# Optimization experiments

Measured on AMD Instinct MI355X. Metric: run time of the kernel, lower is better.

Reference implementation:

```python
import jax, jax.numpy as jnp
import numpy as np
import math

N_EMBED = 8192
EMBD_DIM = 256
B, T = 16, 1024
LN_EPS = 1e-5


def setup_inputs() -> dict:
    key = jax.random.key(0)
    k1, k2 = jax.random.split(key)
    return {
        "input": jax.random.normal(k1, (B, T, EMBD_DIM), dtype=jnp.float32),
        "ln_w": jnp.ones((EMBD_DIM,), dtype=jnp.float32),
        "ln_b": jnp.zeros((EMBD_DIM,), dtype=jnp.float32),
        "embd": jax.random.normal(k2, (N_EMBED, EMBD_DIM), dtype=jnp.float32),
    }


def reference(input, ln_w, ln_b, embd):
    # LayerNorm over last dim (eps matches torch default 1e-5)
    mean = jnp.mean(input, axis=-1, keepdims=True)
    var = jnp.mean(jnp.square(input - mean), axis=-1, keepdims=True)
    x = (input - mean) * jax.lax.rsqrt(var + LN_EPS) * ln_w + ln_b
    # attention-style soft quantization: Q=x, K=V=embd
    scale = 1.0 / math.sqrt(EMBD_DIM)
    logits = jnp.einsum('btd,nd->btn', x, embd) * scale  # [B,T,N]
    probs = jax.nn.softmax(logits, axis=-1)
    idxs = jnp.argmax(probs, axis=-1)  # [B,T]
    quantize = jnp.einsum('btn,nd->btd', probs, embd)  # [B,T,D]
    return (quantize, idxs)
```

## Files before the change

### kernel.cpp

```cpp
#include <hip/hip_runtime.h>
#include <stdint.h>

#define N_EMB 8192
#define M_TOT 16384
#define DELTA 6e-3f
#define LN_EPS 1e-5f
#define SCL 0.09016994f

typedef _Float16 f16;
typedef f16 f16x8 __attribute__((ext_vector_type(8)));
typedef f16 f16x4 __attribute__((ext_vector_type(4)));
typedef float f32x16 __attribute__((ext_vector_type(16)));
typedef unsigned uint32x4 __attribute__((ext_vector_type(4)));

#define WS_KFRAG 0ul
#define WS_VFRAG (4ul << 20)
#define WS_COUNT (8ul << 20)
#define WS_LIST ((8ul << 20) + 64ul)
#define WS_PART (9ul << 20)
#define WS_EMBDT (10ul << 20)

#define MFMA32(a, b, c) __builtin_amdgcn_mfma_f32_32x32x16_f16(a, b, c, 0, 0, 0)
#define SBAR() __builtin_amdgcn_sched_barrier(0)

__global__ __launch_bounds__(256) void prep_kernel(const float* __restrict__ embd,
                                                   f16* __restrict__ kfrag,
                                                   f16* __restrict__ vfrag,
                                                   float* __restrict__ embd_t,
                                                   unsigned* __restrict__ count) {
  const int t = threadIdx.x;
  const int bid = blockIdx.x;
  if (bid < 256) {
    if (bid == 0 && t == 0) *count = 0u;
    __shared__ f16 tile[32][272];
    const int c = bid;
    {
      const int r = t >> 3;
      const int d0 = (t & 7) * 32;
      const float4* src = (const float4*)(embd + (size_t)(c * 32 + r) * 256 + d0);
#pragma unroll
      for (int qd = 0; qd < 8; ++qd) {
        float4 v = src[qd];
        tile[r][d0 + qd * 4 + 0] = (f16)v.x;
        tile[r][d0 + qd * 4 + 1] = (f16)v.y;
        tile[r][d0 + qd * 4 + 2] = (f16)v.z;
        tile[r][d0 + qd * 4 + 3] = (f16)v.w;
      }
    }
    __syncthreads();
#pragma unroll
    for (int i = 0; i < 4; ++i) {
      const int u = t + i * 256;
      const int kc = u >> 6;
      const int l = u & 63;
      const f16x8 pack = *(const f16x8*)&tile[l & 31][kc * 16 + ((l >> 5) & 1) * 8];
      *(f16x8*)(kfrag + (size_t)c * 8192 + (size_t)u * 8) = pack;
    }
#pragma unroll
    for (int i = 0; i < 4; ++i) {
      const int u = t + i * 256;
      const int fi = u >> 6;
      const int l = u & 63;
      const int dt = fi >> 1, ks = fi & 1;
      f16x8 pack;
#pragma unroll
      for (int j = 0; j < 8; ++j)
        pack[j] = tile[ks * 16 + ((l >> 5) & 1) * 8 + j][dt * 32 + (l & 31)];
      *(f16x8*)(vfrag + (size_t)c * 8192 + (size_t)u * 8) = pack;
    }
  } else {
    __shared__ float ftile[32][257];
    const int c = bid - 256;
    {
      const int r = t >> 3;
      const int d0 = (t & 7) * 32;
      const float4* src = (const float4*)(embd + (size_t)(c * 32 + r) * 256 + d0);
#pragma unroll
      for (int q8 = 0; q8 < 8; ++q8) {
        const float4 v = src[q8];
        ftile[r][d0 + q8 * 4 + 0] = v.x;
        ftile[r][d0 + q8 * 4 + 1] = v.y;
        ftile[r][d0 + q8 * 4 + 2] = v.z;
        ftile[r][d0 + q8 * 4 + 3] = v.w;
      }
    }
    __syncthreads();
    const int r = t & 31;
    const int dh = t >> 5;
#pragma unroll
    for (int dd = 0; dd < 32; ++dd) {
      const int d = dd * 8 + dh;
      embd_t[(size_t)d * 8192 + c * 32 + r] = ftile[r][d];
    }
  }
}

__global__ __launch_bounds__(256, 2) void fused_kernel(
    const float* __restrict__ input, const float* __restrict__ ln_w,
    const float* __restrict__ ln_b, const f16* __restrict__ kfrag,
    const f16* __restrict__ vfrag, float* __restrict__ out_q,
    float* __restrict__ out_idx, unsigned* __restrict__ count,
    int* __restrict__ list) {
  __shared__ __align__(16) char lds[36864];
  const int tid = threadIdx.x;
  const int lane = tid & 63;
  const int w = tid >> 6;
  const int q = lane & 31;
  const int hi = lane >> 5;
  const int R0 = blockIdx.x * 32;

  const f16* const kfbase = kfrag + (size_t)(w * 64) * 8192 + (size_t)lane * 8;
  const f16* const vfbase = vfrag + (size_t)(w * 64) * 8192 + (size_t)lane * 8;
  const char* const qb = lds + hi * 512 + q * 16;

  f16x8 kA[8];
#pragma unroll
  for (int f = 0; f < 8; ++f) kA[f] = *(const f16x8*)(kfbase + f * 512);

  {
    const int r = tid >> 3;
    const int seg = tid & 7;
    const float* rowp = input + (size_t)(R0 + r) * 256 + seg * 32;
    float4 xv[8];
    float sm = 0.f, ssq = 0.f;
#pragma unroll
    for (int qd = 0; qd < 8; ++qd) {
      xv[qd] = ((const float4*)rowp)[qd];
      sm += xv[qd].x + xv[qd].y + xv[qd].z + xv[qd].w;
      ssq += xv[qd].x * xv[qd].x + xv[qd].y * xv[qd].y + xv[qd].z * xv[qd].z +
             xv[qd].w * xv[qd].w;
    }
    sm += __shfl_xor(sm, 1);
    sm += __shfl_xor(sm, 2);
    sm += __shfl_xor(sm, 4);
    ssq += __shfl_xor(ssq, 1);
    ssq += __shfl_xor(ssq, 2);
    ssq += __shfl_xor(ssq, 4);
    const float mean = sm * (1.f / 256.f);
    const float var = ssq * (1.f / 256.f) - mean * mean;
    const float rstd = 1.0f / sqrtf(var + LN_EPS);
#pragma unroll
    for (int qd = 0; qd < 8; ++qd) {
      const int d0 = seg * 32 + qd * 4;
      float4 w4 = *(const float4*)(ln_w + d0);
      float4 b4 = *(const float4*)(ln_b + d0);
      f16x4 hv;
      hv[0] = (f16)((((xv[qd].x - mean) * rstd) * w4.x + b4.x) * SCL);
      hv[1] = (f16)((((xv[qd].y - mean) * rstd) * w4.y + b4.y) * SCL);
      hv[2] = (f16)((((xv[qd].z - mean) * rstd) * w4.z + b4.z) * SCL);
      hv[3] = (f16)((((xv[qd].w - mean) * rstd) * w4.w + b4.w) * SCL);
      const int off = (d0 >> 4) * 1024 + ((d0 >> 3) & 1) * 512 + r * 16 + (d0 & 7) * 2;
      *(f16x4*)(lds + off) = hv;
    }
  }
  __syncthreads();

  f32x16 acc[8] = {};
  float m_run = 0.f, l_run = 0.f, mt1 = -3.0e38f, mt2 = -3.0e38f;
  int i1 = 0;

  for (int c = 0; c < 64; ++c) {
    const int nb = w * 2048 + c * 32;
    const f16* const kc_base = kfbase + (size_t)c * 8192;
    const f16* const vc_base = vfbase + (size_t)c * 8192;
    SBAR();
    __builtin_amdgcn_s_barrier();
    SBAR();
    f16x8 kB[8];
#pragma unroll
    for (int f = 0; f < 8; ++f) kB[f] = *(const f16x8*)(kc_base + 4096 + f * 512);
    f32x16 S = {};
#pragma unroll
    for (int kc = 0; kc < 8; ++kc) {
      const f16x8 qf = *(const f16x8*)(qb + kc * 1024);
      S = MFMA32(kA[kc], qf, S);
    }
    f16x8 va[8];
#pragma unroll
    for (int dt = 0; dt < 8; ++dt) va[dt] = *(const f16x8*)(vc_base + dt * 1024);
#pragma unroll
    for (int kc = 0; kc < 8; ++kc) {
      const f16x8 qf = *(const f16x8*)(qb + (8 + kc) * 1024);
      S = MFMA32(kB[kc], qf, S);
    }
    f16x8 vb[8];
#pragma unroll
    for (int dt = 0; dt < 8; ++dt)
      vb[dt] = *(const f16x8*)(vc_base + 512 + dt * 1024);

    const float y0 = fmaxf(fmaxf(S[0], S[1]), fmaxf(S[2], S[3]));
    const float y1 = fmaxf(fmaxf(S[4], S[5]), fmaxf(S[6], S[7]));
    const float y2 = fmaxf(fmaxf(S[8], S[9]), fmaxf(S[10], S[11]));
    const float y3 = fmaxf(fmaxf(S[12], S[13]), fmaxf(S[14], S[15]));
    const float t1h = fmaxf(fmaxf(y0, y1), fmaxf(y2, y3));
    const float o1 = __shfl_xor(t1h, 32);
    const float t1max = fmaxf(t1h, o1);
    if (__any(t1max - m_run > 8.f)) {
      const float mnew = fmaxf(m_run, t1max);
      const float a = exp2f(m_run - mnew);
      l_run *= a;
      m_run = mnew;
      float av[16];
#pragma unroll
      for (int r = 0; r < 16; ++r)
        av[r] = __shfl(a, (r & 3) + 8 * (r >> 2) + hi * 4);
#pragma unroll
      for (int dt = 0; dt < 8; ++dt)
#pragma unroll
        for (int r = 0; r < 16; ++r) acc[dt][r] *= av[r];
    }
    float P[16];
#pragma unroll
    for (int r = 0; r < 16; ++r) P[r] = exp2f(S[r] - m_run);
    unsigned cc[8], xx[8];
#pragma unroll
    for (int i2 = 0; i2 < 8; ++i2) {
      auto pk = __builtin_amdgcn_cvt_pkrtz(P[2 * i2], P[2 * i2 + 1]);
      cc[i2] = __builtin_bit_cast(unsigned, pk);
    }
#pragma unroll
    for (int i2 = 0; i2 < 8; ++i2)
      xx[i2] = (unsigned)__shfl_xor((int)cc[i2], 32);
    uint32x4 u0, u1;
    u0[0] = hi ? xx[2] : cc[0];
    u0[1] = hi ? xx[3] : cc[1];
    u0[2] = hi ? cc[2] : xx[0];
    u0[3] = hi ? cc[3] : xx[1];
    u1[0] = hi ? xx[6] : cc[4];
    u1[1] = hi ? xx[7] : cc[5];
    u1[2] = hi ? cc[6] : xx[4];
    u1[3] = hi ? cc[7] : xx[5];
    const f16x8 pa0 = __builtin_bit_cast(f16x8, u0);
    const f16x8 pa1 = __builtin_bit_cast(f16x8, u1);

#pragma unroll
    for (int dt = 0; dt < 8; ++dt) acc[dt] = MFMA32(pa0, va[dt], acc[dt]);
    {
      const f16* p = kfbase + (size_t)((c + 1) & 63) * 8192;
#pragma unroll
      for (int f = 0; f < 8; ++f) kA[f] = *(const f16x8*)(p + f * 512);
    }
#pragma unroll
    for (int dt = 0; dt < 8; ++dt) acc[dt] = MFMA32(pa1, vb[dt], acc[dt]);

    {
      float ls = 0.f;
#pragma unroll
      for (int j = 0; j < 8; ++j) ls += (float)pa0[j] + (float)pa1[j];
      l_run += ls;

      const int nbh = nb + hi * 4;
      int lih = 27;
#pragma unroll
      for (int r = 14; r >= 0; --r) {
        const int rl = (r & 3) + 8 * (r >> 2);
        lih = (S[r] == t1h) ? rl : lih;
      }
      float t2h = -3.0e38f;
#pragma unroll
      for (int r = 0; r < 16; ++r) {
        const int rl = (r & 3) + 8 * (r >> 2);
        t2h = fmaxf(t2h, (lih == rl) ? -3.0e38f : S[r]);
      }
      const int ti_h = nbh + lih;
      const float o2 = __shfl_xor(t2h, 32);
      const int oi = __shfl_xor(ti_h, 32);
      float t1, t2;
      int ti;
      if (o1 > t1h || (o1 == t1h && oi < ti_h)) {
        t1 = o1; ti = oi; t2 = fmaxf(t1h, o2);
      } else {
        t1 = t1h; ti = ti_h; t2 = fmaxf(t2h, o1);
      }
      if (t1 > mt1) { mt2 = fmaxf(mt1, t2); mt1 = t1; i1 = ti; }
      else { mt2 = fmaxf(mt2, t1); }
    }
  }

  __syncthreads();
  const float lf = l_run + __shfl_xor(l_run, 32);
  float4* statA = (float4*)(lds + 32768);
  int* statB = (int*)(lds + 32768 + 2048);
  if (hi == 0) {
    statA[w * 32 + q] = make_float4(m_run, lf, mt1, mt2);
    statB[w * 32 + q] = i1;
  }
  __syncthreads();
  const float4 s0 = statA[0 * 32 + q];
  const float4 s1 = statA[1 * 32 + q];
  const float4 s2 = statA[2 * 32 + q];
  const float4 s3 = statA[3 * 32 + q];
  const float mstar = fmaxf(fmaxf(s0.x, s1.x), fmaxf(s2.x, s3.x));
  const float lstar = s0.y * exp2f(s0.x - mstar) + s1.y * exp2f(s1.x - mstar) +
                      s2.y * exp2f(s2.x - mstar) + s3.y * exp2f(s3.x - mstar);
  const float a_self = exp2f(m_run - mstar);
  const float inv = 1.0f / lstar;
  if (w == 0 && hi == 0) {
    float wm = s0.z, wm2 = s0.w;
    int wi = statB[q];
    if (s1.z > wm) { wm2 = fmaxf(wm, s1.w); wm = s1.z; wi = statB[32 + q]; }
    else wm2 = fmaxf(wm2, s1.z);
    if (s2.z > wm) { wm2 = fmaxf(wm, s2.w); wm = s2.z; wi = statB[64 + q]; }
    else wm2 = fmaxf(wm2, s2.z);
    if (s3.z > wm) { wm2 = fmaxf(wm, s3.w); wm = s3.z; wi = statB[96 + q]; }
    else wm2 = fmaxf(wm2, s3.z);
    const int row = R0 + q;
    out_idx[row] = (float)wi;
    if (wm - wm2 <= DELTA) {
      const unsigned pos = atomicAdd(count, 1u);
      list[pos] = row;
    }
  }
  float av[16], ivr[16];
#pragma unroll
  for (int r = 0; r < 16; ++r) {
    const int qr = (r & 3) + 8 * (r >> 2) + hi * 4;
    av[r] = __shfl(a_self, qr);
    ivr[r] = __shfl(inv, qr);
  }
#pragma unroll
  for (int dt = 0; dt < 8; ++dt)
#pragma unroll
    for (int r = 0; r < 16; ++r) acc[dt][r] *= av[r];
  __syncthreads();
  float* region = (float*)lds;
#define MRG_ADDR(dt, r) (((r & 3) + 8 * (r >> 2) + hi * 4) * 256 + dt * 32 + q)
  if (w == 1) {
#pragma unroll
    for (int dt = 0; dt < 8; ++dt)
#pragma unroll
      for (int r = 0; r < 16; ++r) region[MRG_ADDR(dt, r)] = acc[dt][r];
  }
  __syncthreads();
  if (w == 0) {
#pragma unroll
    for (int dt = 0; dt < 8; ++dt)
#pragma unroll
      for (int r = 0; r < 16; ++r) acc[dt][r] += region[MRG_ADDR(dt, r)];
  }
  __syncthreads();
  if (w == 3) {
#pragma unroll
    for (int dt = 0; dt < 8; ++dt)
#pragma unroll
      for (int r = 0; r < 16; ++r) region[MRG_ADDR(dt, r)] = acc[dt][r];
  }
  __syncthreads();
  if (w == 2) {
#pragma unroll
    for (int dt = 0; dt < 8; ++dt)
#pragma unroll
      for (int r = 0; r < 16; ++r) acc[dt][r] += region[MRG_ADDR(dt, r)];
  }
  __syncthreads();
  if (w == 2) {
#pragma unroll
    for (int dt = 0; dt < 8; ++dt)
#pragma unroll
      for (int r = 0; r < 16; ++r) region[MRG_ADDR(dt, r)] = acc[dt][r];
  }
  __syncthreads();
  if (w == 0) {
#pragma unroll
    for (int dt = 0; dt < 8; ++dt)
#pragma unroll
      for (int r = 0; r < 16; ++r) {
        const int qr = (r & 3) + 8 * (r >> 2) + hi * 4;
        const float v = (acc[dt][r] + region[MRG_ADDR(dt, r)]) * ivr[r];
        out_q[(size_t)(R0 + qr) * 256 + dt * 32 + q] = v;
      }
  }
#undef MRG_ADDR
}

__global__ __launch_bounds__(256) void refine_part_kernel(
    const float* __restrict__ input, const float* __restrict__ ln_w,
    const float* __restrict__ ln_b, const float* __restrict__ embd_t,
    const unsigned* __restrict__ count, const int* __restrict__ list,
    float2* __restrict__ part) {
  __shared__ float xr[8][256];
  __shared__ float redv[4][8];
  __shared__ int redn[4][8];
  const int tid = threadIdx.x;
  const unsigned cnt = *count;
  if (cnt == 0) return;
  const unsigned ntask = ((cnt + 7u) >> 3) * 8u;
  for (unsigned task = blockIdx.x; task < ntask; task += gridDim.x) {
    const unsigned grp = task >> 3;
    const int slice = (int)(task & 7u);
    __syncthreads();
    {
      const int rr = tid >> 5;
      const int sl = tid & 31;
      unsigned ridx = grp * 8u + (unsigned)rr;
      if (ridx >= cnt) ridx = cnt - 1u;
      const int row = list[ridx];
      const float* rp = input + (size_t)row * 256 + sl * 8;
      const float4 a = ((const float4*)rp)[0];
      const float4 b = ((const float4*)rp)[1];
      float sm = a.x + a.y + a.z + a.w + b.x + b.y + b.z + b.w;
      float ssq = a.x * a.x + a.y * a.y + a.z * a.z + a.w * a.w +
                  b.x * b.x + b.y * b.y + b.z * b.z + b.w * b.w;
#pragma unroll
      for (int mk = 1; mk <= 16; mk <<= 1) {
        sm += __shfl_xor(sm, mk);
        ssq += __shfl_xor(ssq, mk);
      }
      const float mean = sm * (1.f / 256.f);
      const float var = ssq * (1.f / 256.f) - mean * mean;
      const float rstd = 1.0f / sqrtf(var + LN_EPS);
      const float4 w0 = ((const float4*)(ln_w + sl * 8))[0];
      const float4 w1 = ((const float4*)(ln_w + sl * 8))[1];
      const float4 b0 = ((const float4*)(ln_b + sl * 8))[0];
      const float4 b1 = ((const float4*)(ln_b + sl * 8))[1];
      float4 o0, o1;
      o0.x = (a.x - mean) * rstd * w0.x + b0.x;
      o0.y = (a.y - mean) * rstd * w0.y + b0.y;
      o0.z = (a.z - mean) * rstd * w0.z + b0.z;
      o0.w = (a.w - mean) * rstd * w0.w + b0.w;
      o1.x = (b.x - mean) * rstd * w1.x + b1.x;
      o1.y = (b.y - mean) * rstd * w1.y + b1.y;
      o1.z = (b.z - mean) * rstd * w1.z + b1.z;
      o1.w = (b.w - mean) * rstd * w1.w + b1.w;
      *(float4*)&xr[rr][sl * 8] = o0;
      *(float4*)&xr[rr][sl * 8 + 4] = o1;
    }
    __syncthreads();
    const int n0 = slice * 1024 + tid;
    float dv[4][8] = {};
#pragma unroll 2
    for (int dq = 0; dq < 64; ++dq) {
      float4 x[8];
#pragma unroll
      for (int rr = 0; rr < 8; ++rr) x[rr] = *(const float4*)&xr[rr][dq * 4];
      const float* e0 = embd_t + (size_t)(dq * 4 + 0) * 8192 + n0;
      const float* e1 = embd_t + (size_t)(dq * 4 + 1) * 8192 + n0;
      const float* e2 = embd_t + (size_t)(dq * 4 + 2) * 8192 + n0;
      const float* e3 = embd_t + (size_t)(dq * 4 + 3) * 8192 + n0;
#pragma unroll
      for (int k = 0; k < 4; ++k) {
        const float ea = e0[k * 256];
        const float eb = e1[k * 256];
        const float ec = e2[k * 256];
        const float ed = e3[k * 256];
#pragma unroll
        for (int rr = 0; rr < 8; ++rr)
          dv[k][rr] += x[rr].x * ea + x[rr].y * eb + x[rr].z * ec + x[rr].w * ed;
      }
    }
#pragma unroll
    for (int rr = 0; rr < 8; ++rr) {
      float v = dv[0][rr];
      int nn = n0;
#pragma unroll
      for (int k = 1; k < 4; ++k)
        if (dv[k][rr] > v) { v = dv[k][rr]; nn = n0 + k * 256; }
#pragma unroll
      for (int mk = 1; mk <= 32; mk <<= 1) {
        const float ov = __shfl_xor(v, mk);
        const int on = __shfl_xor(nn, mk);
        if (ov > v || (ov == v && on < nn)) { v = ov; nn = on; }
      }
      if ((tid & 63) == 0) {
        redv[tid >> 6][rr] = v;
        redn[tid >> 6][rr] = nn;
      }
    }
    __syncthreads();
    if (tid < 8) {
      const unsigned ridx = grp * 8u + (unsigned)tid;
      if (ridx < cnt) {
        float v = redv[0][tid];
        int nn = redn[0][tid];
#pragma unroll
        for (int wv = 1; wv < 4; ++wv) {
          const float ov = redv[wv][tid];
          const int on = redn[wv][tid];
          if (ov > v || (ov == v && on < nn)) { v = ov; nn = on; }
        }
        part[ridx * 8u + (unsigned)slice] = make_float2(v, (float)nn);
      }
    }
  }
}

__global__ __launch_bounds__(256) void refine_merge_kernel(
    float* __restrict__ out_idx, const unsigned* __restrict__ count,
    const int* __restrict__ list, const float2* __restrict__ part) {
  const unsigned cnt = *count;
  for (unsigned i = blockIdx.x * 256u + threadIdx.x; i < cnt;
       i += gridDim.x * 256u) {
    float v = -3.0e38f;
    int nn = 0;
#pragma unroll
    for (int s = 0; s < 8; ++s) {
      const float2 p = part[i * 8u + (unsigned)s];
      const int on = (int)p.y;
      if (p.x > v || (p.x == v && on < nn)) { v = p.x; nn = on; }
    }
    out_idx[list[i]] = (float)nn;
  }
}

extern "C" void kernel_launch(void* const* d_in, const int* in_sizes, int n_in,
                              void* d_out, int out_size, void* d_ws,
                              size_t ws_size, hipStream_t stream) {
  (void)in_sizes;
  (void)n_in;
  (void)out_size;
  (void)ws_size;
  const float* input = (const float*)d_in[0];
  const float* ln_w = (const float*)d_in[1];
  const float* ln_b = (const float*)d_in[2];
  const float* embd = (const float*)d_in[3];
  float* out_q = (float*)d_out;
  float* out_idx = out_q + (size_t)M_TOT * 256;
  char* ws = (char*)d_ws;
  f16* kfrag = (f16*)(ws + WS_KFRAG);
  f16* vfrag = (f16*)(ws + WS_VFRAG);
  unsigned* count = (unsigned*)(ws + WS_COUNT);
  int* list = (int*)(ws + WS_LIST);
  float2* part = (float2*)(ws + WS_PART);
  float* embd_t = (float*)(ws + WS_EMBDT);

  prep_kernel<<<512, 256, 0, stream>>>(embd, kfrag, vfrag, embd_t, count);
  fused_kernel<<<512, 256, 0, stream>>>(input, ln_w, ln_b, kfrag, vfrag,
                                        out_q, out_idx, count, list);
  refine_part_kernel<<<256, 256, 0, stream>>>(input, ln_w, ln_b, embd_t,
                                              count, list, part);
  refine_merge_kernel<<<16, 256, 0, stream>>>(out_idx, count, list, part);
}
```

Measured before the change: 279.9 us.

## Raise MFMA wave priority and process 16 rows per refine task

Wraps each MFMA block in the main attention loop with s_setprio(1)/s_setprio(0) so matrix waves are favoured by the scheduler over waves doing loads and softmax work. Separately, the fp32 argmax refine kernel now handles 16 candidate rows per task instead of 8, halving the number of tasks and reusing each loaded embedding value across twice as many rows. The refine change raises register use (dv grows to 64 floats) and drops the unroll-2 hint, which may lower occupancy.

Result: slower. 361.8 us (+29.3%).

```diff
diff --git a/kernel.cpp b/kernel.cpp
--- a/kernel.cpp
+++ b/kernel.cpp
@@ -170,19 +170,23 @@
 #pragma unroll
     for (int f = 0; f < 8; ++f) kB[f] = *(const f16x8*)(kc_base + 4096 + f * 512);
     f32x16 S = {};
+    __builtin_amdgcn_s_setprio(1);
 #pragma unroll
     for (int kc = 0; kc < 8; ++kc) {
       const f16x8 qf = *(const f16x8*)(qb + kc * 1024);
       S = MFMA32(kA[kc], qf, S);
     }
+    __builtin_amdgcn_s_setprio(0);
     f16x8 va[8];
 #pragma unroll
     for (int dt = 0; dt < 8; ++dt) va[dt] = *(const f16x8*)(vc_base + dt * 1024);
+    __builtin_amdgcn_s_setprio(1);
 #pragma unroll
     for (int kc = 0; kc < 8; ++kc) {
       const f16x8 qf = *(const f16x8*)(qb + (8 + kc) * 1024);
       S = MFMA32(kB[kc], qf, S);
     }
+    __builtin_amdgcn_s_setprio(0);
     f16x8 vb[8];
 #pragma unroll
     for (int dt = 0; dt < 8; ++dt)
@@ -233,15 +237,19 @@
     const f16x8 pa0 = __builtin_bit_cast(f16x8, u0);
     const f16x8 pa1 = __builtin_bit_cast(f16x8, u1);
 
+    __builtin_amdgcn_s_setprio(1);
 #pragma unroll
     for (int dt = 0; dt < 8; ++dt) acc[dt] = MFMA32(pa0, va[dt], acc[dt]);
+    __builtin_amdgcn_s_setprio(0);
     {
       const f16* p = kfbase + (size_t)((c + 1) & 63) * 8192;
 #pragma unroll
       for (int f = 0; f < 8; ++f) kA[f] = *(const f16x8*)(p + f * 512);
     }
+    __builtin_amdgcn_s_setprio(1);
 #pragma unroll
     for (int dt = 0; dt < 8; ++dt) acc[dt] = MFMA32(pa1, vb[dt], acc[dt]);
+    __builtin_amdgcn_s_setprio(0);
 
     {
       float ls = 0.f;
@@ -378,78 +386,80 @@
     const float* __restrict__ ln_b, const float* __restrict__ embd_t,
     const unsigned* __restrict__ count, const int* __restrict__ list,
     float2* __restrict__ part) {
-  __shared__ float xr[8][256];
-  __shared__ float redv[4][8];
-  __shared__ int redn[4][8];
+  __shared__ float xr[16][256];
+  __shared__ float redv[4][16];
+  __shared__ int redn[4][16];
   const int tid = threadIdx.x;
   const unsigned cnt = *count;
   if (cnt == 0) return;
-  const unsigned ntask = ((cnt + 7u) >> 3) * 8u;
+  const unsigned ntask = ((cnt + 15u) >> 4) * 8u;
   for (unsigned task = blockIdx.x; task < ntask; task += gridDim.x) {
     const unsigned grp = task >> 3;
     const int slice = (int)(task & 7u);
     __syncthreads();
     {
-      const int rr = tid >> 5;
-      const int sl = tid & 31;
-      unsigned ridx = grp * 8u + (unsigned)rr;
+      const int rr = tid >> 4;
+      const int sl = tid & 15;
+      unsigned ridx = grp * 16u + (unsigned)rr;
       if (ridx >= cnt) ridx = cnt - 1u;
       const int row = list[ridx];
-      const float* rp = input + (size_t)row * 256 + sl * 8;
-      const float4 a = ((const float4*)rp)[0];
-      const float4 b = ((const float4*)rp)[1];
-      float sm = a.x + a.y + a.z + a.w + b.x + b.y + b.z + b.w;
-      float ssq = a.x * a.x + a.y * a.y + a.z * a.z + a.w * a.w +
-                  b.x * b.x + b.y * b.y + b.z * b.z + b.w * b.w;
-#pragma unroll
-      for (int mk = 1; mk <= 16; mk <<= 1) {
+      const float* rp = input + (size_t)row * 256 + sl * 16;
+      float4 a[4];
+#pragma unroll
+      for (int j = 0; j < 4; ++j) a[j] = ((const float4*)rp)[j];
+      float sm = 0.f, ssq = 0.f;
+#pragma unroll
+      for (int j = 0; j < 4; ++j) {
+        sm += a[j].x + a[j].y + a[j].z + a[j].w;
+        ssq += a[j].x * a[j].x + a[j].y * a[j].y + a[j].z * a[j].z +
+               a[j].w * a[j].w;
+      }
+#pragma unroll
+      for (int mk = 1; mk <= 8; mk <<= 1) {
         sm += __shfl_xor(sm, mk);
         ssq += __shfl_xor(ssq, mk);
       }
       const float mean = sm * (1.f / 256.f);
       const float var = ssq * (1.f / 256.f) - mean * mean;
       const float rstd = 1.0f / sqrtf(var + LN_EPS);
-      const float4 w0 = ((const float4*)(ln_w + sl * 8))[0];
-      const float4 w1 = ((const float4*)(ln_w + sl * 8))[1];
-      const float4 b0 = ((const float4*)(ln_b + sl * 8))[0];
-      const float4 b1 = ((const float4*)(ln_b + sl * 8))[1];
-      float4 o0, o1;
-      o0.x = (a.x - mean) * rstd * w0.x + b0.x;
-      o0.y = (a.y - mean) * rstd * w0.y + b0.y;
-      o0.z = (a.z - mean) * rstd * w0.z + b0.z;
-      o0.w = (a.w - mean) * rstd * w0.w + b0.w;
-      o1.x = (b.x - mean) * rstd * w1.x + b1.x;
-      o1.y = (b.y - mean) * rstd * w1.y + b1.y;
-      o1.z = (b.z - mean) * rstd * w1.z + b1.z;
-      o1.w = (b.w - mean) * rstd * w1.w + b1.w;
-      *(float4*)&xr[rr][sl * 8] = o0;
-      *(float4*)&xr[rr][sl * 8 + 4] = o1;
+#pragma unroll
+      for (int j = 0; j < 4; ++j) {
+        const float4 w4 = ((const float4*)(ln_w + sl * 16))[j];
+        const float4 b4 = ((const float4*)(ln_b + sl * 16))[j];
+        float4 o;
+        o.x = (a[j].x - mean) * rstd * w4.x + b4.x;
+        o.y = (a[j].y - mean) * rstd * w4.y + b4.y;
+        o.z = (a[j].z - mean) * rstd * w4.z + b4.z;
+        o.w = (a[j].w - mean) * rstd * w4.w + b4.w;
+        *(float4*)&xr[rr][sl * 16 + j * 4] = o;
+      }
     }
     __syncthreads();
     const int n0 = slice * 1024 + tid;
-    float dv[4][8] = {};
-#pragma unroll 2
+    float dv[4][16] = {};
     for (int dq = 0; dq < 64; ++dq) {
-      float4 x[8];
-#pragma unroll
-      for (int rr = 0; rr < 8; ++rr) x[rr] = *(const float4*)&xr[rr][dq * 4];
-      const float* e0 = embd_t + (size_t)(dq * 4 + 0) * 8192 + n0;
-      const float* e1 = embd_t + (size_t)(dq * 4 + 1) * 8192 + n0;
-      const float* e2 = embd_t + (size_t)(dq * 4 + 2) * 8192 + n0;
-      const float* e3 = embd_t + (size_t)(dq * 4 + 3) * 8192 + n0;
-#pragma unroll
-      for (int k = 0; k < 4; ++k) {
-        const float ea = e0[k * 256];
-        const float eb = e1[k * 256];
-        const float ec = e2[k * 256];
-        const float ed = e3[k * 256];
-#pragma unroll
-        for (int rr = 0; rr < 8; ++rr)
-          dv[k][rr] += x[rr].x * ea + x[rr].y * eb + x[rr].z * ec + x[rr].w * ed;
-      }
-    }
-#pragma unroll
-    for (int rr = 0; rr < 8; ++rr) {
+      float e[4][4];
+#pragma unroll
+      for (int ds = 0; ds < 4; ++ds) {
+        const float* ep = embd_t + (size_t)(dq * 4 + ds) * 8192 + n0;
+#pragma unroll
+        for (int k = 0; k < 4; ++k) e[k][ds] = ep[k * 256];
+      }
+#pragma unroll
+      for (int h = 0; h < 2; ++h) {
+        float4 x[8];
+#pragma unroll
+        for (int r8 = 0; r8 < 8; ++r8) x[r8] = *(const float4*)&xr[h * 8 + r8][dq * 4];
+#pragma unroll
+        for (int k = 0; k < 4; ++k)
+#pragma unroll
+          for (int r8 = 0; r8 < 8; ++r8)
+            dv[k][h * 8 + r8] += x[r8].x * e[k][0] + x[r8].y * e[k][1] +
+                                 x[r8].z * e[k][2] + x[r8].w * e[k][3];
+      }
+    }
+#pragma unroll
+    for (int rr = 0; rr < 16; ++rr) {
       float v = dv[0][rr];
       int nn = n0;
 #pragma unroll
@@ -467,8 +477,8 @@
       }
     }
     __syncthreads();
-    if (tid < 8) {
-      const unsigned ridx = grp * 8u + (unsigned)tid;
+    if (tid < 16) {
+      const unsigned ridx = grp * 16u + (unsigned)tid;
       if (ridx < cnt) {
         float v = redv[0][tid];
         int nn = redn[0][tid];
```
